# Kernel tuning notes

Hardware: AMD Instinct MI355X
Metric: run time of the kernel (lower is better)

## Reference

```python
import jax, jax.numpy as jnp
import numpy as np

TEMP = 0.5
ALPHA, BETA, GAMMA, LAMB = 1e-3, 5e-4, 1e-3, 5e-6
IMG = 1024.0  # img_metas img_shape (H_img, W_img)
LN_EPS = 1e-5


def setup_inputs() -> dict:
    key = jax.random.key(0)
    ks = jax.random.split(key, 20)
    N, C, H, W, NB = 8, 256, 128, 128, 20
    preds_S = jax.random.normal(ks[0], (N, C, H, W), jnp.float32)
    preds_T = jax.random.normal(ks[1], (N, C, H, W), jnp.float32)
    # valid boxes (tl_x, tl_y, br_x, br_y) in pixel coords within [0, IMG]
    raw = jax.random.uniform(ks[2], (N, NB, 4), jnp.float32)
    x1 = raw[..., 0] * 0.7 * IMG
    y1 = raw[..., 1] * 0.7 * IMG
    x2 = jnp.minimum(x1 + (0.05 + raw[..., 2] * 0.25) * IMG, IMG)
    y2 = jnp.minimum(y1 + (0.05 + raw[..., 3] * 0.25) * IMG, IMG)
    gt_bboxes = jnp.stack([x1, y1, x2, y2], axis=-1)
    s = 1.0 / np.sqrt(C)
    s2 = 1.0 / np.sqrt(C // 2)
    mk = lambda k, shape, sc: jax.random.normal(k, shape, jnp.float32) * sc
    return {
        'preds_S': preds_S, 'preds_T': preds_T, 'gt_bboxes': gt_bboxes,
        'w_ms': mk(ks[3], (C,), s), 'b_ms': jnp.zeros((), jnp.float32),
        'w_mt': mk(ks[4], (C,), s), 'b_mt': jnp.zeros((), jnp.float32),
        'w1_s': mk(ks[5], (C // 2, C), s), 'b1_s': jnp.zeros((C // 2,), jnp.float32),
        'g_s': jnp.ones((C // 2,), jnp.float32), 'be_s': jnp.zeros((C // 2,), jnp.float32),
        'w2_s': mk(ks[6], (C, C // 2), s2), 'b2_s': jnp.zeros((C,), jnp.float32),
        'w1_t': mk(ks[7], (C // 2, C), s), 'b1_t': jnp.zeros((C // 2,), jnp.float32),
        'g_t': jnp.ones((C // 2,), jnp.float32), 'be_t': jnp.zeros((C // 2,), jnp.float32),
        'w2_t': mk(ks[8], (C, C // 2), s2), 'b2_t': jnp.zeros((C,), jnp.float32),
    }


def _attention(x):
    # x: [N,C,H,W] -> S_att [N,H,W], C_att [N,C]
    N, C, H, W = x.shape
    v = jnp.abs(x)
    fea = v.mean(axis=1)                                   # [N,H,W]
    S = (H * W) * jax.nn.softmax((fea / TEMP).reshape(N, -1), axis=1)
    ch = v.mean(axis=(2, 3))                               # [N,C]
    Ca = C * jax.nn.softmax(ch / TEMP, axis=1)
    return S.reshape(N, H, W), Ca


def _masks(gt, H, W):
    # gt: [N,nb,4] pixel coords; box-rasterized scatter-max foreground mask
    wmin = jnp.floor(gt[..., 0] / IMG * W)
    wmax = jnp.ceil(gt[..., 2] / IMG * W)
    hmin = jnp.floor(gt[..., 1] / IMG * H)
    hmax = jnp.ceil(gt[..., 3] / IMG * H)
    area = 1.0 / ((hmax + 1.0 - hmin) * (wmax + 1.0 - wmin))  # [N,nb]
    hs = jnp.arange(H, dtype=jnp.float32)[None, None, :, None]
    ws = jnp.arange(W, dtype=jnp.float32)[None, None, None, :]
    inb = (hs >= hmin[:, :, None, None]) & (hs <= hmax[:, :, None, None]) \
        & (ws >= wmin[:, :, None, None]) & (ws <= wmax[:, :, None, None])
    Mask_fg = jnp.where(inb, area[:, :, None, None], 0.0).max(axis=1)  # [N,H,W]
    Mask_bg = jnp.where(Mask_fg > 0, 0.0, 1.0)
    sbg = Mask_bg.sum(axis=(1, 2), keepdims=True)
    Mask_bg = jnp.where(sbg > 0, Mask_bg / sbg, Mask_bg)
    return Mask_fg, Mask_bg


def _spatial_pool(x, w, b):
    N, C, H, W = x.shape
    cm = jnp.einsum('nchw,c->nhw', x, w) + b
    sm = jax.nn.softmax(cm.reshape(N, -1), axis=1).reshape(N, H, W)
    return jnp.einsum('nchw,nhw->nc', x, sm)               # [N,C]


def _channel_add(ctx, w1, b1, g, be, w2, b2):
    y = ctx @ w1.T + b1                                    # [N,C/2]
    m = y.mean(axis=1, keepdims=True)
    v = y.var(axis=1, keepdims=True)
    y = (y - m) / jnp.sqrt(v + LN_EPS) * g + be
    y = jax.nn.relu(y)
    return y @ w2.T + b2                                   # [N,C]


def reference(preds_S, preds_T, gt_bboxes, w_ms, b_ms, w_mt, b_mt,
              w1_s, b1_s, g_s, be_s, w2_s, b2_s,
              w1_t, b1_t, g_t, be_t, w2_t, b2_t):
    N, C, H, W = preds_S.shape
    S_t, C_t = _attention(preds_T)
    S_s, C_s = _attention(preds_S)
    Mask_fg, Mask_bg = _masks(gt_bboxes, H, W)
    # feature losses: (fg_s - fg_t) = (S - T) * sqrt(S_t)*sqrt(C_t)*sqrt(mask)
    wgt = jnp.sqrt(S_t)[:, None] * jnp.sqrt(C_t)[:, :, None, None]
    d = (preds_S - preds_T) * wgt
    fg_loss = jnp.sum((d * jnp.sqrt(Mask_fg)[:, None]) ** 2) / N
    bg_loss = jnp.sum((d * jnp.sqrt(Mask_bg)[:, None]) ** 2) / N
    mask_loss = jnp.sum(jnp.abs(C_s - C_t)) / N + jnp.sum(jnp.abs(S_s - S_t)) / N
    ctx_s = _spatial_pool(preds_S, w_ms, b_ms)
    ctx_t = _spatial_pool(preds_T, w_mt, b_mt)
    add_s = _channel_add(ctx_s, w1_s, b1_s, g_s, be_s, w2_s, b2_s)
    add_t = _channel_add(ctx_t, w1_t, b1_t, g_t, be_t, w2_t, b2_t)
    rd = (preds_S + add_s[:, :, None, None]) - (preds_T + add_t[:, :, None, None])
    rela_loss = jnp.sum(rd ** 2) / N
    return ALPHA * fg_loss + BETA * bg_loss + GAMMA * mask_loss + LAMB * rela_loss
```

## Files before the change

kernel.cpp:

```cpp
#include <hip/hip_runtime.h>
#include <math.h>

#define NN    8
#define CC    256
#define HWHW  16384
#define NBOX  20

constexpr float C_ALPHA = 1e-3f, C_BETA = 5e-4f, C_GAMMA = 1e-3f, C_LAMB = 5e-6f;
constexpr float C_LN_EPS = 1e-5f;

#define OFF_FEA_S   0
#define OFF_FEA_T   131072
#define OFF_CM_S    262144
#define OFF_CM_T    393216
#define OFF_MFG     524288
#define OFF_PCHS    655360
#define OFF_PCHT    786432
#define OFF_PD      917504
#define OFF_PCTXS   1048576
#define OFF_PCTXT   1179648
#define OFF_CATT    1310720
#define OFF_CTXS    1312768
#define OFF_CTXT    1314816
#define OFF_DSUM    1316864
#define OFF_STATS   1318912
#define OFF_MXP     1318976
#define OFF_ZP      1319488
#define OFF_BG      1320000
#define OFF_SCAL    1320008
#define OFF_Y       1320016
#define OFF_RELAP   1322064

__device__ __forceinline__ float dpp_wave_sum(float x) {
#define DPPADD(ctrl, rm) \
  x += __int_as_float(__builtin_amdgcn_update_dpp(0, __float_as_int(x), ctrl, rm, 0xf, true));
  DPPADD(0x111, 0xf)
  DPPADD(0x112, 0xf)
  DPPADD(0x114, 0xf)
  DPPADD(0x118, 0xf)
  DPPADD(0x142, 0xa)
  DPPADD(0x143, 0xc)
#undef DPPADD
  return x;
}

__device__ __forceinline__ float dpp_wave_max(float x) {
#define DPPMAX(ctrl, rm) { \
  int r_ = __builtin_amdgcn_update_dpp(__float_as_int(x), __float_as_int(x), ctrl, rm, 0xf, false); \
  x = fmaxf(x, __int_as_float(r_)); }
  DPPMAX(0x111, 0xf)
  DPPMAX(0x112, 0xf)
  DPPMAX(0x114, 0xf)
  DPPMAX(0x118, 0xf)
  DPPMAX(0x142, 0xa)
  DPPMAX(0x143, 0xc)
#undef DPPMAX
  return x;
}

__device__ __forceinline__ float block_sum256(float v, float* sm) {
  int tid = threadIdx.x;
  v = dpp_wave_sum(v);
  if ((tid & 63) == 63) sm[tid >> 6] = v;
  __syncthreads();
  float r = sm[0] + sm[1] + sm[2] + sm[3];
  __syncthreads();
  return r;
}

__device__ __forceinline__ float block_max256(float v, float* sm) {
  int tid = threadIdx.x;
  v = dpp_wave_max(v);
  if ((tid & 63) == 63) sm[tid >> 6] = v;
  __syncthreads();
  float r = fmaxf(fmaxf(sm[0], sm[1]), fmaxf(sm[2], sm[3]));
  __syncthreads();
  return r;
}

__global__ __launch_bounds__(512, 8) void k1_pass1(
    const float* __restrict__ S, const float* __restrict__ T,
    const float* __restrict__ w_ms, const float* __restrict__ w_mt,
    float* __restrict__ ws) {
  int tid = threadIdx.x;
  int lane = tid & 63, sl = tid >> 6;
  int pb = blockIdx.x, cs = blockIdx.y, n = blockIdx.z;
  int pix0 = pb * 256 + lane * 4;
  int ch0 = cs * 128 + sl * 16;

  __shared__ float l_wS[128], l_wT[128];
  __shared__ float f_feaS[256], f_feaT[256], f_cmS[256], f_cmT[256];
  __shared__ float l_chS[128], l_chT[128], l_D[128];
  __shared__ float l_sq[8];

  if (tid < 128) {
    l_wS[tid] = w_ms[cs * 128 + tid];
    l_wT[tid] = w_mt[cs * 128 + tid];
  }
  if (tid < 256) {
    f_feaS[tid] = 0.f; f_feaT[tid] = 0.f; f_cmS[tid] = 0.f; f_cmT[tid] = 0.f;
  }
  __syncthreads();

  const float* baseS = S + (size_t)(n * CC + ch0) * HWHW + pix0;
  const float* baseT = T + (size_t)(n * CC + ch0) * HWHW + pix0;

  float fSx = 0, fSy = 0, fSz = 0, fSw = 0;
  float fTx = 0, fTy = 0, fTz = 0, fTw = 0;
  float cSx = 0, cSy = 0, cSz = 0, cSw = 0;
  float cTx = 0, cTy = 0, cTz = 0, cTw = 0;
  float sq = 0.f;

#pragma unroll 2
  for (int c = 0; c < 16; c++) {
    float4 s4 = *(const float4*)(baseS + (size_t)c * HWHW);
    float4 t4 = *(const float4*)(baseT + (size_t)c * HWHW);
    float asx = fabsf(s4.x), asy = fabsf(s4.y), asz = fabsf(s4.z), asw = fabsf(s4.w);
    float atx = fabsf(t4.x), aty = fabsf(t4.y), atz = fabsf(t4.z), atw = fabsf(t4.w);
    fSx += asx; fSy += asy; fSz += asz; fSw += asw;
    fTx += atx; fTy += aty; fTz += atz; fTw += atw;
    float wS = l_wS[sl * 16 + c], wT = l_wT[sl * 16 + c];
    cSx = fmaf(s4.x, wS, cSx); cSy = fmaf(s4.y, wS, cSy);
    cSz = fmaf(s4.z, wS, cSz); cSw = fmaf(s4.w, wS, cSw);
    cTx = fmaf(t4.x, wT, cTx); cTy = fmaf(t4.y, wT, cTy);
    cTz = fmaf(t4.z, wT, cTz); cTw = fmaf(t4.w, wT, cTw);
    float dx = s4.x - t4.x, dy = s4.y - t4.y, dz = s4.z - t4.z, dw = s4.w - t4.w;
    sq = fmaf(dx, dx, sq); sq = fmaf(dy, dy, sq);
    sq = fmaf(dz, dz, sq); sq = fmaf(dw, dw, sq);
    float chS_p = (asx + asy) + (asz + asw);
    float chT_p = (atx + aty) + (atz + atw);
    float d_p   = (dx + dy) + (dz + dw);
    chS_p = dpp_wave_sum(chS_p);
    chT_p = dpp_wave_sum(chT_p);
    d_p   = dpp_wave_sum(d_p);
    if (lane == 63) {
      l_chS[sl * 16 + c] = chS_p;
      l_chT[sl * 16 + c] = chT_p;
      l_D[sl * 16 + c]   = d_p;
    }
  }

  atomicAdd(&f_feaS[lane * 4 + 0], fSx); atomicAdd(&f_feaS[lane * 4 + 1], fSy);
  atomicAdd(&f_feaS[lane * 4 + 2], fSz); atomicAdd(&f_feaS[lane * 4 + 3], fSw);
  atomicAdd(&f_feaT[lane * 4 + 0], fTx); atomicAdd(&f_feaT[lane * 4 + 1], fTy);
  atomicAdd(&f_feaT[lane * 4 + 2], fTz); atomicAdd(&f_feaT[lane * 4 + 3], fTw);
  atomicAdd(&f_cmS[lane * 4 + 0], cSx); atomicAdd(&f_cmS[lane * 4 + 1], cSy);
  atomicAdd(&f_cmS[lane * 4 + 2], cSz); atomicAdd(&f_cmS[lane * 4 + 3], cSw);
  atomicAdd(&f_cmT[lane * 4 + 0], cTx); atomicAdd(&f_cmT[lane * 4 + 1], cTy);
  atomicAdd(&f_cmT[lane * 4 + 2], cTz); atomicAdd(&f_cmT[lane * 4 + 3], cTw);

  sq = dpp_wave_sum(sq);
  if (lane == 63) l_sq[sl] = sq;
  __syncthreads();

  if (tid < 256) {
    int gp = n * HWHW + pb * 256 + tid;
    atomicAdd(&ws[OFF_FEA_S + gp], f_feaS[tid]);
    atomicAdd(&ws[OFF_FEA_T + gp], f_feaT[tid]);
    atomicAdd(&ws[OFF_CM_S + gp],  f_cmS[tid]);
    atomicAdd(&ws[OFF_CM_T + gp],  f_cmT[tid]);
  }
  if (tid < 128) {
    int bo = (n * CC + cs * 128 + tid) * 64 + pb;
    ws[OFF_PCHS + bo] = l_chS[tid];
    ws[OFF_PCHT + bo] = l_chT[tid];
    ws[OFF_PD + bo]   = l_D[tid];
  }
  if (tid == 0) {
    float t = 0.f;
#pragma unroll
    for (int i = 0; i < 8; i++) t += l_sq[i];
    atomicAdd(&ws[OFF_SCAL + 0], t);
  }
}

__global__ __launch_bounds__(256) void k2_mask(const float* __restrict__ gt,
                                               float* __restrict__ ws) {
  int tid = threadIdx.x;
  int n   = blockIdx.x >> 6;
  int pix = ((blockIdx.x & 63) << 8) | tid;
  float hf = (float)(pix >> 7), wf = (float)(pix & 127);

  __shared__ float bx[NBOX][5];
  __shared__ float l_bg[4];
  if (tid < NBOX) {
    const float* g = gt + (n * NBOX + tid) * 4;
    float wmin = floorf(g[0] * 0.125f);
    float hmin = floorf(g[1] * 0.125f);
    float wmax = ceilf(g[2] * 0.125f);
    float hmax = ceilf(g[3] * 0.125f);
    bx[tid][0] = wmin; bx[tid][1] = hmin; bx[tid][2] = wmax; bx[tid][3] = hmax;
    bx[tid][4] = 1.0f / ((hmax + 1.0f - hmin) * (wmax + 1.0f - wmin));
  }
  __syncthreads();

  float best = 0.f;
#pragma unroll
  for (int b = 0; b < NBOX; b++) {
    bool in = (hf >= bx[b][1]) && (hf <= bx[b][3]) && (wf >= bx[b][0]) && (wf <= bx[b][2]);
    best = in ? fmaxf(best, bx[b][4]) : best;
  }
  ws[OFF_MFG + n * HWHW + pix] = best;

  float bg = (best > 0.f) ? 0.f : 1.f;
  bg = dpp_wave_sum(bg);
  if ((tid & 63) == 63) l_bg[tid >> 6] = bg;
  __syncthreads();
  if (tid == 0) atomicAdd(&ws[OFF_BG + n], l_bg[0] + l_bg[1] + l_bg[2] + l_bg[3]);
}

__global__ __launch_bounds__(256) void kB_stats1(float* __restrict__ ws) {
  int tid = threadIdx.x;
  int pb = blockIdx.x, n = blockIdx.y;
  __shared__ float sm[4];
  int pix0 = pb * 1024 + tid * 4;
  const int   offs[4]   = {OFF_FEA_S, OFF_FEA_T, OFF_CM_S, OFF_CM_T};
  const float scales[4] = {1.0f / 128.0f, 1.0f / 128.0f, 1.0f, 1.0f};
#pragma unroll
  for (int a = 0; a < 4; a++) {
    float4 v = *(const float4*)&ws[offs[a] + n * HWHW + pix0];
    float sc = scales[a];
    v.x *= sc; v.y *= sc; v.z *= sc; v.w *= sc;
    float mx = fmaxf(fmaxf(v.x, v.y), fmaxf(v.z, v.w));
    mx = block_max256(mx, sm);
    float z = expf(v.x - mx) + expf(v.y - mx) + expf(v.z - mx) + expf(v.w - mx);
    z = block_sum256(z, sm);
    if (tid == 0) {
      ws[OFF_MXP + a * 128 + n * 16 + pb] = mx;
      ws[OFF_ZP + a * 128 + n * 16 + pb]  = z;
    }
  }
}

__global__ __launch_bounds__(256) void kC_stats2(float* __restrict__ ws) {
  int tid = threadIdx.x, n = blockIdx.x;
  __shared__ float sm[4];

  float chS = 0.f, chT = 0.f, Dv = 0.f;
  int base = (n * CC + tid) * 64;
#pragma unroll 4
  for (int k = 0; k < 64; k += 4) {
    float4 a = *(const float4*)&ws[OFF_PCHS + base + k];
    float4 b = *(const float4*)&ws[OFF_PCHT + base + k];
    float4 d = *(const float4*)&ws[OFF_PD + base + k];
    chS += (a.x + a.y) + (a.z + a.w);
    chT += (b.x + b.y) + (b.z + b.w);
    Dv  += (d.x + d.y) + (d.z + d.w);
  }
  ws[OFF_DSUM + n * CC + tid] = Dv;

  float lS = chS * (1.0f / 8192.0f), lT = chT * (1.0f / 8192.0f);
  float mS = block_max256(lS, sm);
  float mT = block_max256(lT, sm);
  float eS = expf(lS - mS), eT = expf(lT - mT);
  float ZS = block_sum256(eS, sm);
  float ZT = block_sum256(eT, sm);
  float cattS = (float)CC * eS / ZS;
  float cattT = (float)CC * eT / ZT;
  ws[OFF_CATT + n * CC + tid] = cattT;
  float mml = block_sum256(fabsf(cattS - cattT), sm);
  if (tid == 0) atomicAdd(&ws[OFF_SCAL + 2], mml);

  if (tid < 4) {
    int a = tid;
    float m = -1e30f;
    for (int i = 0; i < 16; i++)
      m = fmaxf(m, ws[OFF_MXP + a * 128 + n * 16 + i]);
    float Z = 0.f;
    for (int i = 0; i < 16; i++)
      Z += ws[OFF_ZP + a * 128 + n * 16 + i] *
           expf(ws[OFF_MXP + a * 128 + n * 16 + i] - m);
    ws[OFF_STATS + n * 8 + 2 * a]     = m;
    ws[OFF_STATS + n * 8 + 2 * a + 1] = Z;
  }
}

__global__ __launch_bounds__(512, 8) void k4_pass2(
    const float* __restrict__ S, const float* __restrict__ T,
    float* __restrict__ ws) {
  int tid = threadIdx.x;
  int lane = tid & 63, sl = tid >> 6;
  int pb = blockIdx.x, cs = blockIdx.y, n = blockIdx.z;
  int pix0 = pb * 256 + lane * 4;
  int ch0 = cs * 128 + sl * 16;

  __shared__ float l_catt[128];
  __shared__ float wcombL[256], smsL[256], smtL[256];
  __shared__ float l_cs[128], l_ct[128], l_c[8];

  if (tid < 128) l_catt[tid] = ws[OFF_CATT + n * CC + cs * 128 + tid];
  if (tid < 64) {
    float mxFS = ws[OFF_STATS + n * 8 + 0], ZFS = ws[OFF_STATS + n * 8 + 1];
    float mxFT = ws[OFF_STATS + n * 8 + 2], ZFT = ws[OFF_STATS + n * 8 + 3];
    float mxCS = ws[OFF_STATS + n * 8 + 4], ZCS = ws[OFF_STATS + n * 8 + 5];
    float mxCT = ws[OFF_STATS + n * 8 + 6], ZCT = ws[OFF_STATS + n * 8 + 7];
    float bgc  = ws[OFF_BG + n];
    int gp = n * HWHW + pb * 256 + tid * 4;
    float4 fS = *(const float4*)&ws[OFF_FEA_S + gp];
    float4 fT = *(const float4*)&ws[OFF_FEA_T + gp];
    float4 cS = *(const float4*)&ws[OFF_CM_S + gp];
    float4 cT = *(const float4*)&ws[OFF_CM_T + gp];
    float4 mf = *(const float4*)&ws[OFF_MFG + gp];
    float macc = 0.f;
    float fSa[4] = {fS.x, fS.y, fS.z, fS.w};
    float fTa[4] = {fT.x, fT.y, fT.z, fT.w};
    float cSa[4] = {cS.x, cS.y, cS.z, cS.w};
    float cTa[4] = {cT.x, cT.y, cT.z, cT.w};
    float mfa[4] = {mf.x, mf.y, mf.z, mf.w};
#pragma unroll
    for (int j = 0; j < 4; j++) {
      float pT = expf(fTa[j] * (1.0f / 128.0f) - mxFT) / ZFT;
      float pS = expf(fSa[j] * (1.0f / 128.0f) - mxFS) / ZFS;
      float Satt = (float)HWHW * pT;
      float mbg = (mfa[j] > 0.f) ? 0.f : ((bgc > 0.f) ? 1.0f / bgc : 1.0f);
      wcombL[tid * 4 + j] = Satt * (C_ALPHA * mfa[j] + C_BETA * mbg);
      smsL[tid * 4 + j] = expf(cSa[j] - mxCS) / ZCS;
      smtL[tid * 4 + j] = expf(cTa[j] - mxCT) / ZCT;
      macc += fabsf(pS - pT);
    }
    macc = dpp_wave_sum(macc);
    if (tid == 63 && cs == 0) atomicAdd(&ws[OFF_SCAL + 2], macc * (float)HWHW);
  }
  __syncthreads();

  float4 sms = *(const float4*)&smsL[lane * 4];
  float4 smt = *(const float4*)&smtL[lane * 4];
  float4 wcb = *(const float4*)&wcombL[lane * 4];

  const float* baseS = S + (size_t)(n * CC + ch0) * HWHW + pix0;
  const float* baseT = T + (size_t)(n * CC + ch0) * HWHW + pix0;

  float awx = 0, awy = 0, awz = 0, aww = 0;
#pragma unroll 2
  for (int c = 0; c < 16; c++) {
    float4 s4 = *(const float4*)(baseS + (size_t)c * HWHW);
    float4 t4 = *(const float4*)(baseT + (size_t)c * HWHW);
    float ca = l_catt[sl * 16 + c];
    float dx = s4.x - t4.x, dy = s4.y - t4.y, dz = s4.z - t4.z, dw = s4.w - t4.w;
    awx = fmaf(dx * dx, ca, awx); awy = fmaf(dy * dy, ca, awy);
    awz = fmaf(dz * dz, ca, awz); aww = fmaf(dw * dw, ca, aww);
    float xs = fmaf(s4.x, sms.x, fmaf(s4.y, sms.y, fmaf(s4.z, sms.z, s4.w * sms.w)));
    float xt = fmaf(t4.x, smt.x, fmaf(t4.y, smt.y, fmaf(t4.z, smt.z, t4.w * smt.w)));
    xs = dpp_wave_sum(xs);
    xt = dpp_wave_sum(xt);
    if (lane == 63) { l_cs[sl * 16 + c] = xs; l_ct[sl * 16 + c] = xt; }
  }

  float contrib = fmaf(awx, wcb.x, fmaf(awy, wcb.y, fmaf(awz, wcb.z, aww * wcb.w)));
  contrib = dpp_wave_sum(contrib);
  if (lane == 63) l_c[sl] = contrib;
  __syncthreads();

  if (tid < 128) {
    int bo = (n * CC + cs * 128 + tid) * 64 + pb;
    ws[OFF_PCTXS + bo] = l_cs[tid];
    ws[OFF_PCTXT + bo] = l_ct[tid];
  }
  if (tid == 0) {
    float t = 0.f;
#pragma unroll
    for (int i = 0; i < 8; i++) t += l_c[i];
    atomicAdd(&ws[OFF_SCAL + 1], t);
  }
}

__global__ __launch_bounds__(256) void k4b_ctxreduce(float* __restrict__ ws) {
  int tid = threadIdx.x, n = blockIdx.x;
  float a = 0.f, b = 0.f;
  int base = (n * CC + tid) * 64;
#pragma unroll 4
  for (int k = 0; k < 64; k += 4) {
    float4 x = *(const float4*)&ws[OFF_PCTXS + base + k];
    float4 y = *(const float4*)&ws[OFF_PCTXT + base + k];
    a += (x.x + x.y) + (x.z + x.w);
    b += (y.x + y.y) + (y.z + y.w);
  }
  ws[OFF_CTXS + n * CC + tid] = a;
  ws[OFF_CTXT + n * CC + tid] = b;
}

__global__ __launch_bounds__(128) void k5a_mlp1(
    const float* __restrict__ w1_s, const float* __restrict__ b1_s,
    const float* __restrict__ g_s,  const float* __restrict__ be_s,
    const float* __restrict__ w1_t, const float* __restrict__ b1_t,
    const float* __restrict__ g_t,  const float* __restrict__ be_t,
    float* __restrict__ ws) {
  int tid = threadIdx.x;
  int n = blockIdx.x >> 1, st = blockIdx.x & 1;
  const float* w1 = st ? w1_t : w1_s;
  const float* b1 = st ? b1_t : b1_s;
  const float* g  = st ? g_t  : g_s;
  const float* be = st ? be_t : be_s;
  int ctxoff = (st ? OFF_CTXT : OFF_CTXS) + n * CC;

  __shared__ float ctx[CC];
  __shared__ float red[2];
  ctx[tid]       = ws[ctxoff + tid];
  ctx[tid + 128] = ws[ctxoff + tid + 128];
  __syncthreads();

  float acc = b1[tid];
  const float* wr = w1 + tid * CC;
#pragma unroll 8
  for (int c = 0; c < CC; c += 4) {
    float4 w = *(const float4*)(wr + c);
    acc = fmaf(w.x, ctx[c], acc);
    acc = fmaf(w.y, ctx[c + 1], acc);
    acc = fmaf(w.z, ctx[c + 2], acc);
    acc = fmaf(w.w, ctx[c + 3], acc);
  }

  float v = dpp_wave_sum(acc);
  if ((tid & 63) == 63) red[tid >> 6] = v;
  __syncthreads();
  float mean = (red[0] + red[1]) * (1.0f / 128.0f);
  __syncthreads();
  float dm = acc - mean;
  v = dpp_wave_sum(dm * dm);
  if ((tid & 63) == 63) red[tid >> 6] = v;
  __syncthreads();
  float var = (red[0] + red[1]) * (1.0f / 128.0f);
  float q = dm * (1.0f / sqrtf(var + C_LN_EPS)) * g[tid] + be[tid];
  ws[OFF_Y + blockIdx.x * 128 + tid] = q > 0.f ? q : 0.f;
}

__global__ __launch_bounds__(256) void k5b_mlp2(
    const float* __restrict__ w2_s, const float* __restrict__ b2_s,
    const float* __restrict__ w2_t, const float* __restrict__ b2_t,
    float* __restrict__ ws) {
  int tid = threadIdx.x, n = blockIdx.x;
  __shared__ float ysh[128], yth[128];
  __shared__ float sm[4];
  if (tid < 128) ysh[tid] = ws[OFF_Y + (n * 2 + 0) * 128 + tid];
  else           yth[tid - 128] = ws[OFF_Y + (n * 2 + 1) * 128 + (tid - 128)];
  __syncthreads();

  float es = b2_s[tid], et = b2_t[tid];
  const float* w2sr = w2_s + tid * 128;
  const float* w2tr = w2_t + tid * 128;
#pragma unroll 8
  for (int j = 0; j < 128; j += 4) {
    float4 a = *(const float4*)(w2sr + j);
    float4 b = *(const float4*)(w2tr + j);
    es = fmaf(a.x, ysh[j], es); es = fmaf(a.y, ysh[j + 1], es);
    es = fmaf(a.z, ysh[j + 2], es); es = fmaf(a.w, ysh[j + 3], es);
    et = fmaf(b.x, yth[j], et); et = fmaf(b.y, yth[j + 1], et);
    et = fmaf(b.z, yth[j + 2], et); et = fmaf(b.w, yth[j + 3], et);
  }
  float e = es - et;
  float rp = 2.0f * e * ws[OFF_DSUM + n * CC + tid] + (float)HWHW * e * e;
  rp = block_sum256(rp, sm);
  if (tid == 0) ws[OFF_RELAP + n] = rp;
}

__global__ __launch_bounds__(64) void k5c_final(float* __restrict__ ws,
                                                float* __restrict__ out) {
  int lane = threadIdx.x;
  float r = (lane < NN) ? ws[OFF_RELAP + lane] : 0.f;
  r = dpp_wave_sum(r);
  if (lane == 63) {
    float rela = ws[OFF_SCAL + 0] + r;
    out[0] = (ws[OFF_SCAL + 1] + C_GAMMA * ws[OFF_SCAL + 2] + C_LAMB * rela) *
             (1.0f / (float)NN);
  }
}

extern "C" void kernel_launch(void* const* d_in, const int* in_sizes, int n_in,
                              void* d_out, int out_size, void* d_ws, size_t ws_size,
                              hipStream_t stream) {
  const float* S    = (const float*)d_in[0];
  const float* T    = (const float*)d_in[1];
  const float* gt   = (const float*)d_in[2];
  const float* w_ms = (const float*)d_in[3];
  const float* w_mt = (const float*)d_in[5];
  const float* w1_s = (const float*)d_in[7];
  const float* b1_s = (const float*)d_in[8];
  const float* g_s  = (const float*)d_in[9];
  const float* be_s = (const float*)d_in[10];
  const float* w2_s = (const float*)d_in[11];
  const float* b2_s = (const float*)d_in[12];
  const float* w1_t = (const float*)d_in[13];
  const float* b1_t = (const float*)d_in[14];
  const float* g_t  = (const float*)d_in[15];
  const float* be_t = (const float*)d_in[16];
  const float* w2_t = (const float*)d_in[17];
  const float* b2_t = (const float*)d_in[18];
  float* ws = (float*)d_ws;
  float* out = (float*)d_out;

  hipMemsetAsync(ws, 0, 524288 * sizeof(float), stream);
  hipMemsetAsync(ws + OFF_BG, 0, 16 * sizeof(float), stream);

  k1_pass1<<<dim3(64, 2, 8), dim3(512), 0, stream>>>(S, T, w_ms, w_mt, ws);
  k2_mask<<<dim3(512), dim3(256), 0, stream>>>(gt, ws);
  kB_stats1<<<dim3(16, 8), dim3(256), 0, stream>>>(ws);
  kC_stats2<<<dim3(8), dim3(256), 0, stream>>>(ws);
  k4_pass2<<<dim3(64, 2, 8), dim3(512), 0, stream>>>(S, T, ws);
  k4b_ctxreduce<<<dim3(8), dim3(256), 0, stream>>>(ws);
  k5a_mlp1<<<dim3(16), dim3(128), 0, stream>>>(w1_s, b1_s, g_s, be_s,
                                               w1_t, b1_t, g_t, be_t, ws);
  k5b_mlp2<<<dim3(8), dim3(256), 0, stream>>>(w2_s, b2_s, w2_t, b2_t, ws);
  k5c_final<<<dim3(1), dim3(64), 0, stream>>>(ws, out);
}
```

Baseline: 447.9 us.

## Drop global atomics and memset, fuse mask with stats, batch loads in passes

```diff
diff --git a/kernel.cpp b/kernel.cpp
--- a/kernel.cpp
+++ b/kernel.cpp
@@ -5,31 +5,30 @@
 #define CC    256
 #define HWHW  16384
 #define NBOX  20
+#define HALF  131072
 
 constexpr float C_ALPHA = 1e-3f, C_BETA = 5e-4f, C_GAMMA = 1e-3f, C_LAMB = 5e-6f;
 constexpr float C_LN_EPS = 1e-5f;
 
 #define OFF_FEA_S   0
-#define OFF_FEA_T   131072
-#define OFF_CM_S    262144
-#define OFF_CM_T    393216
-#define OFF_MFG     524288
-#define OFF_PCHS    655360
-#define OFF_PCHT    786432
-#define OFF_PD      917504
-#define OFF_PCTXS   1048576
-#define OFF_PCTXT   1179648
-#define OFF_CATT    1310720
-#define OFF_CTXS    1312768
-#define OFF_CTXT    1314816
-#define OFF_DSUM    1316864
-#define OFF_STATS   1318912
-#define OFF_MXP     1318976
-#define OFF_ZP      1319488
-#define OFF_BG      1320000
-#define OFF_SCAL    1320008
-#define OFF_Y       1320016
-#define OFF_RELAP   1322064
+#define OFF_FEA_T   262144
+#define OFF_CM_S    524288
+#define OFF_CM_T    786432
+#define OFF_MFG     1048576
+#define OFF_PCHS    1179648
+#define OFF_PCHT    1310720
+#define OFF_PD      1441792
+#define OFF_PCTXS   1572864
+#define OFF_PCTXT   1703936
+#define OFF_CATT    1835008
+#define OFF_DSUM    1837056
+#define OFF_STATS   1839104
+#define OFF_MXP     1839168
+#define OFF_ZP      1839680
+#define OFF_BG      1840192
+#define OFF_SCAL    1840200
+#define OFF_Y       1840208
+#define OFF_RELAP   1842256
 
 __device__ __forceinline__ float dpp_wave_sum(float x) {
 #define DPPADD(ctrl, rm) \
@@ -78,7 +77,7 @@
   return r;
 }
 
-__global__ __launch_bounds__(512, 8) void k1_pass1(
+__global__ __launch_bounds__(512, 4) void k1_pass1(
     const float* __restrict__ S, const float* __restrict__ T,
     const float* __restrict__ w_ms, const float* __restrict__ w_mt,
     float* __restrict__ ws) {
@@ -105,60 +104,76 @@
   const float* baseS = S + (size_t)(n * CC + ch0) * HWHW + pix0;
   const float* baseT = T + (size_t)(n * CC + ch0) * HWHW + pix0;
 
-  float fSx = 0, fSy = 0, fSz = 0, fSw = 0;
-  float fTx = 0, fTy = 0, fTz = 0, fTw = 0;
-  float cSx = 0, cSy = 0, cSz = 0, cSw = 0;
-  float cTx = 0, cTy = 0, cTz = 0, cTw = 0;
+  float fS[4] = {0.f, 0.f, 0.f, 0.f}, fT[4] = {0.f, 0.f, 0.f, 0.f};
+  float cS[4] = {0.f, 0.f, 0.f, 0.f}, cT[4] = {0.f, 0.f, 0.f, 0.f};
+  float chS_l[16], chT_l[16], D_l[16];
   float sq = 0.f;
 
-#pragma unroll 2
+#define PROC1(c, s4, t4) { \
+    float asx = fabsf(s4.x), asy = fabsf(s4.y), asz = fabsf(s4.z), asw = fabsf(s4.w); \
+    float atx = fabsf(t4.x), aty = fabsf(t4.y), atz = fabsf(t4.z), atw = fabsf(t4.w); \
+    fS[0] += asx; fS[1] += asy; fS[2] += asz; fS[3] += asw; \
+    fT[0] += atx; fT[1] += aty; fT[2] += atz; fT[3] += atw; \
+    chS_l[c] = (asx + asy) + (asz + asw); \
+    chT_l[c] = (atx + aty) + (atz + atw); \
+    float wS = l_wS[sl * 16 + (c)], wT = l_wT[sl * 16 + (c)]; \
+    cS[0] = fmaf(s4.x, wS, cS[0]); cS[1] = fmaf(s4.y, wS, cS[1]); \
+    cS[2] = fmaf(s4.z, wS, cS[2]); cS[3] = fmaf(s4.w, wS, cS[3]); \
+    cT[0] = fmaf(t4.x, wT, cT[0]); cT[1] = fmaf(t4.y, wT, cT[1]); \
+    cT[2] = fmaf(t4.z, wT, cT[2]); cT[3] = fmaf(t4.w, wT, cT[3]); \
+    float dx = s4.x - t4.x, dy = s4.y - t4.y, dz = s4.z - t4.z, dw = s4.w - t4.w; \
+    sq = fmaf(dx, dx, sq); sq = fmaf(dy, dy, sq); \
+    sq = fmaf(dz, dz, sq); sq = fmaf(dw, dw, sq); \
+    D_l[c] = (dx + dy) + (dz + dw); }
+
+#pragma unroll
+  for (int cg = 0; cg < 4; cg++) {
+    float4 s0 = *(const float4*)(baseS + (size_t)(cg * 4 + 0) * HWHW);
+    float4 s1 = *(const float4*)(baseS + (size_t)(cg * 4 + 1) * HWHW);
+    float4 s2 = *(const float4*)(baseS + (size_t)(cg * 4 + 2) * HWHW);
+    float4 s3 = *(const float4*)(baseS + (size_t)(cg * 4 + 3) * HWHW);
+    float4 t0 = *(const float4*)(baseT + (size_t)(cg * 4 + 0) * HWHW);
+    float4 t1 = *(const float4*)(baseT + (size_t)(cg * 4 + 1) * HWHW);
+    float4 t2 = *(const float4*)(baseT + (size_t)(cg * 4 + 2) * HWHW);
+    float4 t3 = *(const float4*)(baseT + (size_t)(cg * 4 + 3) * HWHW);
+    PROC1(cg * 4 + 0, s0, t0)
+    PROC1(cg * 4 + 1, s1, t1)
+    PROC1(cg * 4 + 2, s2, t2)
+    PROC1(cg * 4 + 3, s3, t3)
+  }
+#undef PROC1
+
+#pragma unroll
   for (int c = 0; c < 16; c++) {
-    float4 s4 = *(const float4*)(baseS + (size_t)c * HWHW);
-    float4 t4 = *(const float4*)(baseT + (size_t)c * HWHW);
-    float asx = fabsf(s4.x), asy = fabsf(s4.y), asz = fabsf(s4.z), asw = fabsf(s4.w);
-    float atx = fabsf(t4.x), aty = fabsf(t4.y), atz = fabsf(t4.z), atw = fabsf(t4.w);
-    fSx += asx; fSy += asy; fSz += asz; fSw += asw;
-    fTx += atx; fTy += aty; fTz += atz; fTw += atw;
-    float wS = l_wS[sl * 16 + c], wT = l_wT[sl * 16 + c];
-    cSx = fmaf(s4.x, wS, cSx); cSy = fmaf(s4.y, wS, cSy);
-    cSz = fmaf(s4.z, wS, cSz); cSw = fmaf(s4.w, wS, cSw);
-    cTx = fmaf(t4.x, wT, cTx); cTy = fmaf(t4.y, wT, cTy);
-    cTz = fmaf(t4.z, wT, cTz); cTw = fmaf(t4.w, wT, cTw);
-    float dx = s4.x - t4.x, dy = s4.y - t4.y, dz = s4.z - t4.z, dw = s4.w - t4.w;
-    sq = fmaf(dx, dx, sq); sq = fmaf(dy, dy, sq);
-    sq = fmaf(dz, dz, sq); sq = fmaf(dw, dw, sq);
-    float chS_p = (asx + asy) + (asz + asw);
-    float chT_p = (atx + aty) + (atz + atw);
-    float d_p   = (dx + dy) + (dz + dw);
-    chS_p = dpp_wave_sum(chS_p);
-    chT_p = dpp_wave_sum(chT_p);
-    d_p   = dpp_wave_sum(d_p);
+    float a = dpp_wave_sum(chS_l[c]);
+    float b = dpp_wave_sum(chT_l[c]);
+    float d = dpp_wave_sum(D_l[c]);
     if (lane == 63) {
-      l_chS[sl * 16 + c] = chS_p;
-      l_chT[sl * 16 + c] = chT_p;
-      l_D[sl * 16 + c]   = d_p;
+      l_chS[sl * 16 + c] = a;
+      l_chT[sl * 16 + c] = b;
+      l_D[sl * 16 + c]   = d;
     }
   }
 
-  atomicAdd(&f_feaS[lane * 4 + 0], fSx); atomicAdd(&f_feaS[lane * 4 + 1], fSy);
-  atomicAdd(&f_feaS[lane * 4 + 2], fSz); atomicAdd(&f_feaS[lane * 4 + 3], fSw);
-  atomicAdd(&f_feaT[lane * 4 + 0], fTx); atomicAdd(&f_feaT[lane * 4 + 1], fTy);
-  atomicAdd(&f_feaT[lane * 4 + 2], fTz); atomicAdd(&f_feaT[lane * 4 + 3], fTw);
-  atomicAdd(&f_cmS[lane * 4 + 0], cSx); atomicAdd(&f_cmS[lane * 4 + 1], cSy);
-  atomicAdd(&f_cmS[lane * 4 + 2], cSz); atomicAdd(&f_cmS[lane * 4 + 3], cSw);
-  atomicAdd(&f_cmT[lane * 4 + 0], cTx); atomicAdd(&f_cmT[lane * 4 + 1], cTy);
-  atomicAdd(&f_cmT[lane * 4 + 2], cTz); atomicAdd(&f_cmT[lane * 4 + 3], cTw);
+  atomicAdd(&f_feaS[lane * 4 + 0], fS[0]); atomicAdd(&f_feaS[lane * 4 + 1], fS[1]);
+  atomicAdd(&f_feaS[lane * 4 + 2], fS[2]); atomicAdd(&f_feaS[lane * 4 + 3], fS[3]);
+  atomicAdd(&f_feaT[lane * 4 + 0], fT[0]); atomicAdd(&f_feaT[lane * 4 + 1], fT[1]);
+  atomicAdd(&f_feaT[lane * 4 + 2], fT[2]); atomicAdd(&f_feaT[lane * 4 + 3], fT[3]);
+  atomicAdd(&f_cmS[lane * 4 + 0], cS[0]); atomicAdd(&f_cmS[lane * 4 + 1], cS[1]);
+  atomicAdd(&f_cmS[lane * 4 + 2], cS[2]); atomicAdd(&f_cmS[lane * 4 + 3], cS[3]);
+  atomicAdd(&f_cmT[lane * 4 + 0], cT[0]); atomicAdd(&f_cmT[lane * 4 + 1], cT[1]);
+  atomicAdd(&f_cmT[lane * 4 + 2], cT[2]); atomicAdd(&f_cmT[lane * 4 + 3], cT[3]);
 
   sq = dpp_wave_sum(sq);
   if (lane == 63) l_sq[sl] = sq;
   __syncthreads();
 
   if (tid < 256) {
-    int gp = n * HWHW + pb * 256 + tid;
-    atomicAdd(&ws[OFF_FEA_S + gp], f_feaS[tid]);
-    atomicAdd(&ws[OFF_FEA_T + gp], f_feaT[tid]);
-    atomicAdd(&ws[OFF_CM_S + gp],  f_cmS[tid]);
-    atomicAdd(&ws[OFF_CM_T + gp],  f_cmT[tid]);
+    int gp = cs * HALF + n * HWHW + pb * 256 + tid;
+    ws[OFF_FEA_S + gp] = f_feaS[tid];
+    ws[OFF_FEA_T + gp] = f_feaT[tid];
+    ws[OFF_CM_S + gp]  = f_cmS[tid];
+    ws[OFF_CM_T + gp]  = f_cmT[tid];
   }
   if (tid < 128) {
     int bo = (n * CC + cs * 128 + tid) * 64 + pb;
@@ -174,15 +189,16 @@
   }
 }
 
-__global__ __launch_bounds__(256) void k2_mask(const float* __restrict__ gt,
-                                               float* __restrict__ ws) {
+__global__ __launch_bounds__(256) void k2B_maskstats(const float* __restrict__ gt,
+                                                     float* __restrict__ ws) {
   int tid = threadIdx.x;
-  int n   = blockIdx.x >> 6;
-  int pix = ((blockIdx.x & 63) << 8) | tid;
-  float hf = (float)(pix >> 7), wf = (float)(pix & 127);
+  int pbB = blockIdx.x, n = blockIdx.y;
+  int pix0 = pbB * 1024 + tid * 4;
 
   __shared__ float bx[NBOX][5];
   __shared__ float l_bg[4];
+  __shared__ float sm[4];
+
   if (tid < NBOX) {
     const float* g = gt + (n * NBOX + tid) * 4;
     float wmin = floorf(g[0] * 0.125f);
@@ -194,40 +210,47 @@
   }
   __syncthreads();
 
-  float best = 0.f;
+  float best[4] = {0.f, 0.f, 0.f, 0.f};
 #pragma unroll
   for (int b = 0; b < NBOX; b++) {
-    bool in = (hf >= bx[b][1]) && (hf <= bx[b][3]) && (wf >= bx[b][0]) && (wf <= bx[b][2]);
-    best = in ? fmaxf(best, bx[b][4]) : best;
-  }
-  ws[OFF_MFG + n * HWHW + pix] = best;
-
-  float bg = (best > 0.f) ? 0.f : 1.f;
+    float wmin = bx[b][0], hmin = bx[b][1], wmax = bx[b][2], hmax = bx[b][3];
+    float ar = bx[b][4];
+#pragma unroll
+    for (int j = 0; j < 4; j++) {
+      int pix = pix0 + j;
+      float hf = (float)(pix >> 7), wf = (float)(pix & 127);
+      bool in = (hf >= hmin) && (hf <= hmax) && (wf >= wmin) && (wf <= wmax);
+      best[j] = in ? fmaxf(best[j], ar) : best[j];
+    }
+  }
+  float4 bo;
+  bo.x = best[0]; bo.y = best[1]; bo.z = best[2]; bo.w = best[3];
+  *(float4*)&ws[OFF_MFG + n * HWHW + pix0] = bo;
+
+  float bg = (best[0] > 0.f ? 0.f : 1.f) + (best[1] > 0.f ? 0.f : 1.f) +
+             (best[2] > 0.f ? 0.f : 1.f) + (best[3] > 0.f ? 0.f : 1.f);
   bg = dpp_wave_sum(bg);
   if ((tid & 63) == 63) l_bg[tid >> 6] = bg;
   __syncthreads();
   if (tid == 0) atomicAdd(&ws[OFF_BG + n], l_bg[0] + l_bg[1] + l_bg[2] + l_bg[3]);
-}
-
-__global__ __launch_bounds__(256) void kB_stats1(float* __restrict__ ws) {
-  int tid = threadIdx.x;
-  int pb = blockIdx.x, n = blockIdx.y;
-  __shared__ float sm[4];
-  int pix0 = pb * 1024 + tid * 4;
+
+  int gp = n * HWHW + pix0;
   const int   offs[4]   = {OFF_FEA_S, OFF_FEA_T, OFF_CM_S, OFF_CM_T};
   const float scales[4] = {1.0f / 128.0f, 1.0f / 128.0f, 1.0f, 1.0f};
 #pragma unroll
   for (int a = 0; a < 4; a++) {
-    float4 v = *(const float4*)&ws[offs[a] + n * HWHW + pix0];
+    float4 v0 = *(const float4*)&ws[offs[a] + gp];
+    float4 v1 = *(const float4*)&ws[offs[a] + HALF + gp];
     float sc = scales[a];
-    v.x *= sc; v.y *= sc; v.z *= sc; v.w *= sc;
-    float mx = fmaxf(fmaxf(v.x, v.y), fmaxf(v.z, v.w));
+    float vx = (v0.x + v1.x) * sc, vy = (v0.y + v1.y) * sc;
+    float vz = (v0.z + v1.z) * sc, vw = (v0.w + v1.w) * sc;
+    float mx = fmaxf(fmaxf(vx, vy), fmaxf(vz, vw));
     mx = block_max256(mx, sm);
-    float z = expf(v.x - mx) + expf(v.y - mx) + expf(v.z - mx) + expf(v.w - mx);
+    float z = expf(vx - mx) + expf(vy - mx) + expf(vz - mx) + expf(vw - mx);
     z = block_sum256(z, sm);
     if (tid == 0) {
-      ws[OFF_MXP + a * 128 + n * 16 + pb] = mx;
-      ws[OFF_ZP + a * 128 + n * 16 + pb]  = z;
+      ws[OFF_MXP + a * 128 + n * 16 + pbB] = mx;
+      ws[OFF_ZP + a * 128 + n * 16 + pbB]  = z;
     }
   }
 }
@@ -275,7 +298,7 @@
   }
 }
 
-__global__ __launch_bounds__(512, 8) void k4_pass2(
+__global__ __launch_bounds__(512, 4) void k4_pass2(
     const float* __restrict__ S, const float* __restrict__ T,
     float* __restrict__ ws) {
   int tid = threadIdx.x;
@@ -296,17 +319,21 @@
     float mxCT = ws[OFF_STATS + n * 8 + 6], ZCT = ws[OFF_STATS + n * 8 + 7];
     float bgc  = ws[OFF_BG + n];
     int gp = n * HWHW + pb * 256 + tid * 4;
-    float4 fS = *(const float4*)&ws[OFF_FEA_S + gp];
-    float4 fT = *(const float4*)&ws[OFF_FEA_T + gp];
-    float4 cS = *(const float4*)&ws[OFF_CM_S + gp];
-    float4 cT = *(const float4*)&ws[OFF_CM_T + gp];
+    float4 fS0 = *(const float4*)&ws[OFF_FEA_S + gp];
+    float4 fS1 = *(const float4*)&ws[OFF_FEA_S + HALF + gp];
+    float4 fT0 = *(const float4*)&ws[OFF_FEA_T + gp];
+    float4 fT1 = *(const float4*)&ws[OFF_FEA_T + HALF + gp];
+    float4 cS0 = *(const float4*)&ws[OFF_CM_S + gp];
+    float4 cS1 = *(const float4*)&ws[OFF_CM_S + HALF + gp];
+    float4 cT0 = *(const float4*)&ws[OFF_CM_T + gp];
+    float4 cT1 = *(const float4*)&ws[OFF_CM_T + HALF + gp];
     float4 mf = *(const float4*)&ws[OFF_MFG + gp];
+    float fSa[4] = {fS0.x + fS1.x, fS0.y + fS1.y, fS0.z + fS1.z, fS0.w + fS1.w};
+    float fTa[4] = {fT0.x + fT1.x, fT0.y + fT1.y, fT0.z + fT1.z, fT0.w + fT1.w};
+    float cSa[4] = {cS0.x + cS1.x, cS0.y + cS1.y, cS0.z + cS1.z, cS0.w + cS1.w};
+    float cTa[4] = {cT0.x + cT1.x, cT0.y + cT1.y, cT0.z + cT1.z, cT0.w + cT1.w};
+    float mfa[4] = {mf.x, mf.y, mf.z, mf.w};
     float macc = 0.f;
-    float fSa[4] = {fS.x, fS.y, fS.z, fS.w};
-    float fTa[4] = {fT.x, fT.y, fT.z, fT.w};
-    float cSa[4] = {cS.x, cS.y, cS.z, cS.w};
-    float cTa[4] = {cT.x, cT.y, cT.z, cT.w};
-    float mfa[4] = {mf.x, mf.y, mf.z, mf.w};
 #pragma unroll
     for (int j = 0; j < 4; j++) {
       float pT = expf(fTa[j] * (1.0f / 128.0f) - mxFT) / ZFT;
@@ -330,23 +357,42 @@
   const float* baseS = S + (size_t)(n * CC + ch0) * HWHW + pix0;
   const float* baseT = T + (size_t)(n * CC + ch0) * HWHW + pix0;
 
-  float awx = 0, awy = 0, awz = 0, aww = 0;
-#pragma unroll 2
+  float aw[4] = {0.f, 0.f, 0.f, 0.f};
+  float ctxS_l[16], ctxT_l[16];
+
+#define PROC2(c, s4, t4) { \
+    float ca = l_catt[sl * 16 + (c)]; \
+    float dx = s4.x - t4.x, dy = s4.y - t4.y, dz = s4.z - t4.z, dw = s4.w - t4.w; \
+    aw[0] = fmaf(dx * dx, ca, aw[0]); aw[1] = fmaf(dy * dy, ca, aw[1]); \
+    aw[2] = fmaf(dz * dz, ca, aw[2]); aw[3] = fmaf(dw * dw, ca, aw[3]); \
+    ctxS_l[c] = fmaf(s4.x, sms.x, fmaf(s4.y, sms.y, fmaf(s4.z, sms.z, s4.w * sms.w))); \
+    ctxT_l[c] = fmaf(t4.x, smt.x, fmaf(t4.y, smt.y, fmaf(t4.z, smt.z, t4.w * smt.w))); }
+
+#pragma unroll
+  for (int cg = 0; cg < 4; cg++) {
+    float4 s0 = *(const float4*)(baseS + (size_t)(cg * 4 + 0) * HWHW);
+    float4 s1 = *(const float4*)(baseS + (size_t)(cg * 4 + 1) * HWHW);
+    float4 s2 = *(const float4*)(baseS + (size_t)(cg * 4 + 2) * HWHW);
+    float4 s3 = *(const float4*)(baseS + (size_t)(cg * 4 + 3) * HWHW);
+    float4 t0 = *(const float4*)(baseT + (size_t)(cg * 4 + 0) * HWHW);
+    float4 t1 = *(const float4*)(baseT + (size_t)(cg * 4 + 1) * HWHW);
+    float4 t2 = *(const float4*)(baseT + (size_t)(cg * 4 + 2) * HWHW);
+    float4 t3 = *(const float4*)(baseT + (size_t)(cg * 4 + 3) * HWHW);
+    PROC2(cg * 4 + 0, s0, t0)
+    PROC2(cg * 4 + 1, s1, t1)
+    PROC2(cg * 4 + 2, s2, t2)
+    PROC2(cg * 4 + 3, s3, t3)
+  }
+#undef PROC2
+
+#pragma unroll
   for (int c = 0; c < 16; c++) {
-    float4 s4 = *(const float4*)(baseS + (size_t)c * HWHW);
-    float4 t4 = *(const float4*)(baseT + (size_t)c * HWHW);
-    float ca = l_catt[sl * 16 + c];
-    float dx = s4.x - t4.x, dy = s4.y - t4.y, dz = s4.z - t4.z, dw = s4.w - t4.w;
-    awx = fmaf(dx * dx, ca, awx); awy = fmaf(dy * dy, ca, awy);
-    awz = fmaf(dz * dz, ca, awz); aww = fmaf(dw * dw, ca, aww);
-    float xs = fmaf(s4.x, sms.x, fmaf(s4.y, sms.y, fmaf(s4.z, sms.z, s4.w * sms.w)));
-    float xt = fmaf(t4.x, smt.x, fmaf(t4.y, smt.y, fmaf(t4.z, smt.z, t4.w * smt.w)));
-    xs = dpp_wave_sum(xs);
-    xt = dpp_wave_sum(xt);
+    float xs = dpp_wave_sum(ctxS_l[c]);
+    float xt = dpp_wave_sum(ctxT_l[c]);
     if (lane == 63) { l_cs[sl * 16 + c] = xs; l_ct[sl * 16 + c] = xt; }
   }
 
-  float contrib = fmaf(awx, wcb.x, fmaf(awy, wcb.y, fmaf(awz, wcb.z, aww * wcb.w)));
+  float contrib = fmaf(aw[0], wcb.x, fmaf(aw[1], wcb.y, fmaf(aw[2], wcb.z, aw[3] * wcb.w)));
   contrib = dpp_wave_sum(contrib);
   if (lane == 63) l_c[sl] = contrib;
   __syncthreads();
@@ -362,21 +408,6 @@
     for (int i = 0; i < 8; i++) t += l_c[i];
     atomicAdd(&ws[OFF_SCAL + 1], t);
   }
-}
-
-__global__ __launch_bounds__(256) void k4b_ctxreduce(float* __restrict__ ws) {
-  int tid = threadIdx.x, n = blockIdx.x;
-  float a = 0.f, b = 0.f;
-  int base = (n * CC + tid) * 64;
-#pragma unroll 4
-  for (int k = 0; k < 64; k += 4) {
-    float4 x = *(const float4*)&ws[OFF_PCTXS + base + k];
-    float4 y = *(const float4*)&ws[OFF_PCTXT + base + k];
-    a += (x.x + x.y) + (x.z + x.w);
-    b += (y.x + y.y) + (y.z + y.w);
-  }
-  ws[OFF_CTXS + n * CC + tid] = a;
-  ws[OFF_CTXT + n * CC + tid] = b;
 }
 
 __global__ __launch_bounds__(128) void k5a_mlp1(
@@ -391,12 +422,22 @@
   const float* b1 = st ? b1_t : b1_s;
   const float* g  = st ? g_t  : g_s;
   const float* be = st ? be_t : be_s;
-  int ctxoff = (st ? OFF_CTXT : OFF_CTXS) + n * CC;
+  int pbase = (st ? OFF_PCTXT : OFF_PCTXS) + n * CC * 64;
 
   __shared__ float ctx[CC];
   __shared__ float red[2];
-  ctx[tid]       = ws[ctxoff + tid];
-  ctx[tid + 128] = ws[ctxoff + tid + 128];
+#pragma unroll
+  for (int half = 0; half < 2; half++) {
+    int c = tid + half * 128;
+    const float* p = ws + pbase + c * 64;
+    float a = 0.f;
+#pragma unroll 4
+    for (int k = 0; k < 64; k += 4) {
+      float4 x = *(const float4*)(p + k);
+      a += (x.x + x.y) + (x.z + x.w);
+    }
+    ctx[c] = a;
+  }
   __syncthreads();
 
   float acc = b1[tid];
@@ -488,15 +529,12 @@
   float* ws = (float*)d_ws;
   float* out = (float*)d_out;
 
-  hipMemsetAsync(ws, 0, 524288 * sizeof(float), stream);
   hipMemsetAsync(ws + OFF_BG, 0, 16 * sizeof(float), stream);
 
   k1_pass1<<<dim3(64, 2, 8), dim3(512), 0, stream>>>(S, T, w_ms, w_mt, ws);
-  k2_mask<<<dim3(512), dim3(256), 0, stream>>>(gt, ws);
-  kB_stats1<<<dim3(16, 8), dim3(256), 0, stream>>>(ws);
+  k2B_maskstats<<<dim3(16, 8), dim3(256), 0, stream>>>(gt, ws);
   kC_stats2<<<dim3(8), dim3(256), 0, stream>>>(ws);
   k4_pass2<<<dim3(64, 2, 8), dim3(512), 0, stream>>>(S, T, ws);
-  k4b_ctxreduce<<<dim3(8), dim3(256), 0, stream>>>(ws);
   k5a_mlp1<<<dim3(16), dim3(128), 0, stream>>>(w1_s, b1_s, g_s, be_s,
                                                w1_t, b1_t, g_t, be_t, ws);
   k5b_mlp2<<<dim3(8), dim3(256), 0, stream>>>(w2_s, b2_s, w2_t, b2_t, ws);
```

New measurement: 577.4 us. 1.29x slower.
